# Kernel optimization log

Measured on AMD Instinct MI355X. Metric: run time of the kernel, lower is better.

## Reference

```python
import jax, jax.numpy as jnp
import numpy as np

LN_EPS = 1e-5


def setup_inputs() -> dict:
    key = jax.random.key(0)
    ks = jax.random.split(key, 6)
    n_nodes, mem_dim = 500000, 256
    n_upd, msg_dim = 65536, 512
    return {
        "unique_node_ids": jnp.arange(n_upd, dtype=jnp.int64) if jax.config.jax_enable_x64 else jnp.arange(n_upd, dtype=jnp.int32),
        "unique_messages": jax.random.normal(ks[0], (n_upd, msg_dim), dtype=jnp.float32),
        "timestamps": jax.random.uniform(ks[1], (n_upd,), dtype=jnp.float32),
        "memory": jax.random.normal(ks[2], (n_nodes, mem_dim), dtype=jnp.float32),
        "last_update": jnp.zeros((n_nodes,), dtype=jnp.float32),
        "W_ih": jax.random.normal(ks[3], (3 * mem_dim, msg_dim), dtype=jnp.float32) * (1.0 / np.sqrt(msg_dim)),
        "W_hh": jax.random.normal(ks[4], (3 * mem_dim, mem_dim), dtype=jnp.float32) * (1.0 / np.sqrt(mem_dim)),
        "b_ih": jnp.zeros((3 * mem_dim,), dtype=jnp.float32),
        "b_hh": jnp.zeros((3 * mem_dim,), dtype=jnp.float32),
        "ln_gamma": jnp.ones((mem_dim,), dtype=jnp.float32),
        "ln_beta": jnp.zeros((mem_dim,), dtype=jnp.float32),
    }


def _gru_cell(x, h, W_ih, W_hh, b_ih, b_hh):
    # torch.nn.GRUCell math
    gi = x @ W_ih.T + b_ih          # [N, 3H]
    gh = h @ W_hh.T + b_hh          # [N, 3H]
    i_r, i_z, i_n = jnp.split(gi, 3, axis=-1)
    h_r, h_z, h_n = jnp.split(gh, 3, axis=-1)
    r = jax.nn.sigmoid(i_r + h_r)
    z = jax.nn.sigmoid(i_z + h_z)
    n = jnp.tanh(i_n + r * h_n)
    return (1.0 - z) * n + z * h


def _layer_norm(x, gamma, beta):
    mu = jnp.mean(x, axis=-1, keepdims=True)
    var = jnp.mean(jnp.square(x - mu), axis=-1, keepdims=True)
    return (x - mu) * jax.lax.rsqrt(var + LN_EPS) * gamma + beta


def reference(unique_node_ids, unique_messages, timestamps, memory, last_update,
              W_ih, W_hh, b_ih, b_hh, ln_gamma, ln_beta):
    # gather memory rows for the nodes being updated
    h = memory[unique_node_ids]                      # [N, H]
    new_h = _gru_cell(unique_messages, h, W_ih, W_hh, b_ih, b_hh)
    new_h = _layer_norm(new_h, ln_gamma, ln_beta)
    # scatter updated rows back (get_updated_memory semantics: pure copy)
    updated_memory = memory.at[unique_node_ids].set(new_h)
    updated_last_update = last_update.at[unique_node_ids].set(timestamps)
    return updated_memory, updated_last_update
```

## Files before the change

kernel.cpp:

```cpp
#include <hip/hip_runtime.h>
#include <hip/hip_bf16.h>

typedef float  f32x4 __attribute__((ext_vector_type(4)));
typedef short  s16x8 __attribute__((ext_vector_type(8)));

#define MEMH   256
#define MSGD   512
#define G3     768
#define W_IH_ELEMS (G3*MSGD)
#define W_HH_ELEMS (G3*MEMH)
#define W_TOT_ELEMS (W_IH_ELEMS + W_HH_ELEMS)
#define W_BYTES    ((size_t)W_TOT_ELEMS * 2)

#define BM     32
#define NTHR   1024
#define AM_OFF 0
#define AH_OFF 32768
#define PART_OFF 49152
#define CNT_OFF  51200
#define LDS_BYTES 51264

static __device__ __forceinline__ short f2bf(float x) {
    __hip_bfloat16 b = __float2bfloat16(x);
    return __builtin_bit_cast(short, b);
}
static __device__ __forceinline__ float bf2f(short s) {
    unsigned int u = ((unsigned int)(unsigned short)s) << 16;
    return __builtin_bit_cast(float, u);
}
static __device__ __forceinline__ float sigf(float x) {
    return 1.f / (1.f + __expf(-x));
}
static __device__ __forceinline__ float tanh_fast(float x) {
    float e = __expf(-2.f * fabsf(x));
    float t = (1.f - e) / (1.f + e);
    return copysignf(t, x);
}
static __device__ __forceinline__ f32x4 ntload4(const float* p) {
    return __builtin_nontemporal_load((const f32x4*)p);
}
static __device__ __forceinline__ void ntstore4(float* p, f32x4 v) {
    __builtin_nontemporal_store(v, (f32x4*)p);
}

__global__ void smu_copy_kernel(const float* __restrict__ mem,
                                const float* __restrict__ lu,
                                float* __restrict__ out_mem,
                                float* __restrict__ out_lu,
                                long n_mem4, long n_lu4) {
    long i = (long)blockIdx.x * blockDim.x + threadIdx.x;
    long stride = (long)gridDim.x * blockDim.x;
    long total = n_mem4 + n_lu4;
    for (; i < total; i += stride) {
        if (i < n_mem4) ntstore4(out_mem + i * 4, ntload4(mem + i * 4));
        else {
            long j = (i - n_mem4) * 4;
            ntstore4(out_lu + j, ntload4(lu + j));
        }
    }
}

__global__ void smu_cvtw_kernel(const float* __restrict__ wih,
                                const float* __restrict__ whh,
                                short* __restrict__ o) {
    int i = blockIdx.x * blockDim.x + threadIdx.x;
    if (i >= W_TOT_ELEMS) return;
    if (i < W_IH_ELEMS) {
        int f = i >> 9, r = i & 511, l = r >> 3, e = r & 7;
        int t = f >> 4, k = f & 15;
        int row = t * 16 + (l & 15), col = k * 32 + (l >> 4) * 8 + e;
        o[i] = f2bf(wih[row * MSGD + col]);
    } else {
        int j = i - W_IH_ELEMS;
        int f = j >> 9, r = j & 511, l = r >> 3, e = r & 7;
        int t = f >> 3, k = f & 7;
        int row = t * 16 + (l & 15), col = k * 32 + (l >> 4) * 8 + e;
        o[i] = f2bf(whh[row * MEMH + col]);
    }
}

__global__ void smu_clear_kernel(unsigned* __restrict__ p, int n) {
    int i = blockIdx.x * blockDim.x + threadIdx.x;
    if (i < n) p[i] = 0u;
}
__global__ void smu_bits_kernel(const int* __restrict__ ids,
                                unsigned* __restrict__ bm, int n) {
    int i = blockIdx.x * blockDim.x + threadIdx.x;
    if (i < n) {
        int id = ids[i];
        atomicOr(&bm[id >> 5], 1u << (id & 31));
    }
}

template<bool USE_WS>
static __device__ __forceinline__ s16x8 load_b(const float* __restrict__ Wf,
                                               const short* __restrict__ Wb,
                                               int t, int k, int ldk, int nkt, int lane) {
    if constexpr (USE_WS) {
        return *(const s16x8*)(Wb + ((size_t)(t * nkt + k) << 9) + lane * 8);
    } else {
        int row = t * 16 + (lane & 15);
        int col = k * 32 + (lane >> 4) * 8;
        f32x4 x = *(const f32x4*)(Wf + (size_t)row * ldk + col);
        f32x4 y = *(const f32x4*)(Wf + (size_t)row * ldk + col + 4);
        s16x8 s;
        s[0]=f2bf(x[0]); s[1]=f2bf(x[1]); s[2]=f2bf(x[2]); s[3]=f2bf(x[3]);
        s[4]=f2bf(y[0]); s[5]=f2bf(y[1]); s[6]=f2bf(y[2]); s[7]=f2bf(y[3]);
        return s;
    }
}

template<bool USE_WS, bool FUSED>
__global__ __launch_bounds__(NTHR, 1)
void smu_fused_kernel(const int*   __restrict__ ids,
                      const float* __restrict__ msg,
                      const float* __restrict__ ts,
                      const float* __restrict__ memory,
                      const float* __restrict__ lu,
                      const float* __restrict__ W_ih,
                      const float* __restrict__ W_hh,
                      const float* __restrict__ b_ih,
                      const float* __restrict__ b_hh,
                      const float* __restrict__ gamma,
                      const float* __restrict__ beta,
                      const short* __restrict__ wsw,
                      const unsigned* __restrict__ bm,
                      float* __restrict__ out_mem,
                      float* __restrict__ out_lu,
                      long n_nodes) {
    __shared__ __align__(16) unsigned char lds[LDS_BYTES];
    const int tid = threadIdx.x;
    const int bid = blockIdx.x;
    const long base = (long)bid * BM;

    if (tid == 0) *(unsigned*)(lds + CNT_OFF) = 0u;

    {
        const float* src = msg + base * MSGD;
        #pragma unroll
        for (int it = 0; it < 2; ++it) {
            int u = tid + NTHR * it;
            int row = u >> 6;
            f32x4 a = ntload4(src + u * 8);
            f32x4 b = ntload4(src + u * 8 + 4);
            s16x8 s;
            s[0]=f2bf(a[0]); s[1]=f2bf(a[1]); s[2]=f2bf(a[2]); s[3]=f2bf(a[3]);
            s[4]=f2bf(b[0]); s[5]=f2bf(b[1]); s[6]=f2bf(b[2]); s[7]=f2bf(b[3]);
            int byte = AM_OFF + ((u * 16) ^ ((row & 7) << 4));
            *(s16x8*)(lds + byte) = s;
        }
        {
            int u = tid;
            int row = u >> 5;
            int c8  = u & 31;
            int id  = ids[base + row];
            const float* hs = memory + (size_t)id * MEMH + c8 * 8;
            f32x4 a = ntload4(hs);
            f32x4 b = ntload4(hs + 4);
            s16x8 s;
            s[0]=f2bf(a[0]); s[1]=f2bf(a[1]); s[2]=f2bf(a[2]); s[3]=f2bf(a[3]);
            s[4]=f2bf(b[0]); s[5]=f2bf(b[1]); s[6]=f2bf(b[2]); s[7]=f2bf(b[3]);
            int byte = AH_OFF + ((u * 16) ^ ((row & 7) << 4));
            *(s16x8*)(lds + byte) = s;
        }
    }
    __syncthreads();

    if (tid >= 512) {
        if constexpr (FUSED) {
            const long nu     = n_nodes * (MEMH / 4);
            const long stride = (long)gridDim.x * 512;
            const long i0     = (long)bid * 512 + (tid - 512);

            for (long i = i0; i < nu; i += stride * 8) {
                f32x4 v[8];
                bool  f[8];
                #pragma unroll
                for (int j = 0; j < 8; ++j) {
                    long u = i + stride * j;
                    f[j] = false;
                    if (u < nu) {
                        long r = u >> 6;
                        f[j] = !((bm[r >> 5] >> (r & 31)) & 1u);
                        if (f[j]) v[j] = ntload4(memory + u * 4);
                    }
                }
                #pragma unroll
                for (int j = 0; j < 8; ++j) {
                    long u = i + stride * j;
                    if (f[j]) ntstore4(out_mem + u * 4, v[j]);
                }
            }
            for (long i = i0; i < n_nodes; i += stride) {
                if (!((bm[i >> 5] >> (i & 31)) & 1u)) {
                    float v = __builtin_nontemporal_load(lu + i);
                    __builtin_nontemporal_store(v, out_lu + i);
                }
            }
        }
        return;
    }

    const int lane = tid & 63;
    const int w    = tid >> 6;
    const int lr   = lane & 15;
    const int lk8  = (lane >> 4) * 8;
    const int sw   = (lr & 7) << 4;
    const short* Wi = wsw;
    const short* Wh = wsw + W_IH_ELEMS;

    f32x4 rz[2][2][2] = {};
    f32x4 gin[2][2]   = {};
    f32x4 ghn[2][2]   = {};

    {
        s16x8 b[2][6];
        #pragma unroll
        for (int i = 0; i < 6; ++i)
            b[0][i] = load_b<USE_WS>(W_ih, Wi, w + 8*(i/3) + 16*(i%3), 0, MSGD, 16, lane);
        #pragma unroll
        for (int i = 0; i < 6; ++i)
            b[1][i] = load_b<USE_WS>(W_ih, Wi, w + 8*(i/3) + 16*(i%3), 1, MSGD, 16, lane);
        #pragma unroll
        for (int k = 0; k < 16; ++k) {
            const int cb = (k * 32 + lk8) * 2;
            #pragma unroll
            for (int m = 0; m < 2; ++m) {
                s16x8 a = *(const s16x8*)(lds + AM_OFF + (((m*16 + lr) * 1024 + cb) ^ sw));
                #pragma unroll
                for (int ci = 0; ci < 2; ++ci) {
                    rz[m][ci][0] = __builtin_amdgcn_mfma_f32_16x16x32_bf16(a, b[k & 1][ci*3+0], rz[m][ci][0], 0, 0, 0);
                    rz[m][ci][1] = __builtin_amdgcn_mfma_f32_16x16x32_bf16(a, b[k & 1][ci*3+1], rz[m][ci][1], 0, 0, 0);
                    gin[m][ci]   = __builtin_amdgcn_mfma_f32_16x16x32_bf16(a, b[k & 1][ci*3+2], gin[m][ci],   0, 0, 0);
                }
            }
            if (k < 14) {
                #pragma unroll
                for (int i = 0; i < 6; ++i)
                    b[k & 1][i] = load_b<USE_WS>(W_ih, Wi, w + 8*(i/3) + 16*(i%3), k + 2, MSGD, 16, lane);
            }
        }
    }
    {
        s16x8 b[2][6];
        #pragma unroll
        for (int i = 0; i < 6; ++i)
            b[0][i] = load_b<USE_WS>(W_hh, Wh, w + 8*(i/3) + 16*(i%3), 0, MEMH, 8, lane);
        #pragma unroll
        for (int i = 0; i < 6; ++i)
            b[1][i] = load_b<USE_WS>(W_hh, Wh, w + 8*(i/3) + 16*(i%3), 1, MEMH, 8, lane);
        #pragma unroll
        for (int k = 0; k < 8; ++k) {
            const int cb = (k * 32 + lk8) * 2;
            #pragma unroll
            for (int m = 0; m < 2; ++m) {
                s16x8 a = *(const s16x8*)(lds + AH_OFF + (((m*16 + lr) * 512 + cb) ^ sw));
                #pragma unroll
                for (int ci = 0; ci < 2; ++ci) {
                    rz[m][ci][0] = __builtin_amdgcn_mfma_f32_16x16x32_bf16(a, b[k & 1][ci*3+0], rz[m][ci][0], 0, 0, 0);
                    rz[m][ci][1] = __builtin_amdgcn_mfma_f32_16x16x32_bf16(a, b[k & 1][ci*3+1], rz[m][ci][1], 0, 0, 0);
                    ghn[m][ci]   = __builtin_amdgcn_mfma_f32_16x16x32_bf16(a, b[k & 1][ci*3+2], ghn[m][ci],   0, 0, 0);
                }
            }
            if (k < 6) {
                #pragma unroll
                for (int i = 0; i < 6; ++i)
                    b[k & 1][i] = load_b<USE_WS>(W_hh, Wh, w + 8*(i/3) + 16*(i%3), k + 2, MEMH, 8, lane);
            }
        }
    }

    const int lq = (lane >> 4);
    f32x4 o_[2][2];
    {
        #pragma unroll
        for (int ci = 0; ci < 2; ++ci) {
            const int j = (w + 8*ci) * 16 + lr;
            const float br = b_ih[j]       + b_hh[j];
            const float bz = b_ih[256 + j] + b_hh[256 + j];
            const float bihn = b_ih[512 + j], bhhn = b_hh[512 + j];
            #pragma unroll
            for (int m = 0; m < 2; ++m) {
                #pragma unroll
                for (int q = 0; q < 4; ++q) {
                    int row = m * 16 + lq * 4 + q;
                    float r = sigf(rz[m][ci][0][q] + br);
                    float z = sigf(rz[m][ci][1][q] + bz);
                    float n = tanh_fast(gin[m][ci][q] + bihn + r * (ghn[m][ci][q] + bhhn));
                    float hv = bf2f(*(const short*)(lds + AH_OFF + ((row * 512 + j * 2) ^ ((row & 7) << 4))));
                    o_[m][ci][q] = (1.f - z) * n + z * hv;
                }
            }
        }
    }

    {
        float* part = (float*)(lds + PART_OFF);
        #pragma unroll
        for (int m = 0; m < 2; ++m) {
            #pragma unroll
            for (int q = 0; q < 4; ++q) {
                float v0 = o_[m][0][q], v1 = o_[m][1][q];
                float s1 = v0 + v1;
                float s2 = v0 * v0 + v1 * v1;
                #pragma unroll
                for (int mk = 1; mk < 16; mk <<= 1) {
                    s1 += __shfl_xor(s1, mk);
                    s2 += __shfl_xor(s2, mk);
                }
                if (lr == 0) {
                    int row = m * 16 + lq * 4 + q;
                    part[(row * 8 + w) * 2]     = s1;
                    part[(row * 8 + w) * 2 + 1] = s2;
                }
            }
        }
    }

    __threadfence_block();
    if (lane == 0) atomicAdd((unsigned*)(lds + CNT_OFF), 1u);
    {
        volatile unsigned* cp = (volatile unsigned*)(lds + CNT_OFF);
        while (*cp < 8u) __builtin_amdgcn_s_sleep(2);
    }
    __threadfence_block();

    float mu_[2][4], inv_[2][4];
    {
        const float* part = (const float*)(lds + PART_OFF);
        #pragma unroll
        for (int m = 0; m < 2; ++m) {
            #pragma unroll
            for (int q = 0; q < 4; ++q) {
                int row = m * 16 + lq * 4 + q;
                float s1 = 0.f, s2 = 0.f;
                #pragma unroll
                for (int i = 0; i < 8; ++i) {
                    s1 += part[(row * 8 + i) * 2];
                    s2 += part[(row * 8 + i) * 2 + 1];
                }
                float mu  = s1 * (1.f / 256.f);
                float var = fmaxf(s2 * (1.f / 256.f) - mu * mu, 0.f);
                mu_[m][q]  = mu;
                inv_[m][q] = rsqrtf(var + 1e-5f);
            }
        }
    }

    {
        #pragma unroll
        for (int ci = 0; ci < 2; ++ci) {
            const int j = (w + 8*ci) * 16 + lr;
            const float ga = gamma[j], be = beta[j];
            #pragma unroll
            for (int m = 0; m < 2; ++m) {
                #pragma unroll
                for (int q = 0; q < 4; ++q) {
                    int row = m * 16 + lq * 4 + q;
                    int id = ids[base + row];
                    float y = (o_[m][ci][q] - mu_[m][q]) * inv_[m][q] * ga + be;
                    __builtin_nontemporal_store(y, out_mem + (size_t)id * MEMH + j);
                }
            }
        }
        if (w == 0 && lane < 32) {
            int id = ids[base + lane];
            __builtin_nontemporal_store(ts[base + lane], out_lu + id);
        }
    }
}

extern "C" void kernel_launch(void* const* d_in, const int* in_sizes, int n_in,
                              void* d_out, int out_size, void* d_ws, size_t ws_size,
                              hipStream_t stream) {
    (void)n_in; (void)out_size;
    const int*   ids = (const int*)  d_in[0];
    const float* msg = (const float*)d_in[1];
    const float* ts  = (const float*)d_in[2];
    const float* mem = (const float*)d_in[3];
    const float* lu  = (const float*)d_in[4];
    const float* Wih = (const float*)d_in[5];
    const float* Whh = (const float*)d_in[6];
    const float* bih = (const float*)d_in[7];
    const float* bhh = (const float*)d_in[8];
    const float* gam = (const float*)d_in[9];
    const float* bet = (const float*)d_in[10];

    const int  n_upd   = in_sizes[0];
    const long n_nodes = (long)in_sizes[3] / MEMH;

    float* out_mem = (float*)d_out;
    float* out_lu  = out_mem + (size_t)n_nodes * MEMH;

    const int    bm_words     = (int)((n_nodes + 31) / 32) + 4;
    const size_t bm_bytes_pad = (size_t)bm_words * 4;
    const bool ws_w  = (d_ws != nullptr) && (ws_size >= W_BYTES);
    const bool ws_bm = (d_ws != nullptr) && (ws_size >= W_BYTES + bm_bytes_pad);

    short*    wsw = (short*)d_ws;
    unsigned* bm  = (unsigned*)((char*)d_ws + W_BYTES);

    const int grid = n_upd / BM;

    if (ws_w) {
        smu_cvtw_kernel<<<(W_TOT_ELEMS + 255) / 256, 256, 0, stream>>>(Wih, Whh, wsw);
    }

    if (ws_bm) {
        smu_clear_kernel<<<(bm_words + 255) / 256, 256, 0, stream>>>(bm, bm_words);
        smu_bits_kernel<<<(n_upd + 255) / 256, 256, 0, stream>>>(ids, bm, n_upd);
        smu_fused_kernel<true, true><<<grid, NTHR, 0, stream>>>(
            ids, msg, ts, mem, lu, Wih, Whh, bih, bhh, gam, bet,
            wsw, bm, out_mem, out_lu, n_nodes);
    } else {
        long n_mem4 = n_nodes * (MEMH / 4);
        long n_lu4  = n_nodes / 4;
        smu_copy_kernel<<<2048, 256, 0, stream>>>(mem, lu, out_mem, out_lu, n_mem4, n_lu4);
        if (ws_w) {
            smu_fused_kernel<true, false><<<grid, NTHR, 0, stream>>>(
                ids, msg, ts, mem, lu, Wih, Whh, bih, bhh, gam, bet,
                wsw, nullptr, out_mem, out_lu, n_nodes);
        } else {
            smu_fused_kernel<false, false><<<grid, NTHR, 0, stream>>>(
                ids, msg, ts, mem, lu, Wih, Whh, bih, bhh, gam, bet,
                nullptr, nullptr, out_mem, out_lu, n_nodes);
        }
    }
}
```

Baseline: 377.9 us.

## Split fused copy+GRU kernel into separate bitmap-skip copy and GRU kernels

Removes the warp-specialized design where half of each 1024-thread block streamed the untouched memory rows while the other half ran the GRU. The copy now runs in its own grid-stride kernel that skips rows flagged in the bitmap, followed by a 512-thread GRU kernel allowing several blocks per CU. The LDS spin-wait counter is replaced by a plain __syncthreads. This trades the overlap of copy and compute for simpler scheduling and higher GRU occupancy, at the cost of serializing the bandwidth-bound copy before the compute.

Result: faster. 341.3 us (-9.7%).

```diff
diff --git a/kernel.cpp b/kernel.cpp
--- a/kernel.cpp
+++ b/kernel.cpp
@@ -13,12 +13,11 @@
 #define W_BYTES    ((size_t)W_TOT_ELEMS * 2)
 
 #define BM     32
-#define NTHR   1024
+#define NTHR   512
 #define AM_OFF 0
 #define AH_OFF 32768
 #define PART_OFF 49152
-#define CNT_OFF  51200
-#define LDS_BYTES 51264
+#define LDS_BYTES 51200
 
 static __device__ __forceinline__ short f2bf(float x) {
     __hip_bfloat16 b = __float2bfloat16(x);
@@ -56,6 +55,30 @@
         else {
             long j = (i - n_mem4) * 4;
             ntstore4(out_lu + j, ntload4(lu + j));
+        }
+    }
+}
+
+__global__ __launch_bounds__(256)
+void smu_copy_skip_kernel(const float* __restrict__ mem,
+                          const float* __restrict__ lu,
+                          const unsigned* __restrict__ bm,
+                          float* __restrict__ out_mem,
+                          float* __restrict__ out_lu,
+                          long n_nodes) {
+    const long nu = n_nodes * (MEMH / 4);
+    const long stride = (long)gridDim.x * blockDim.x;
+    const long i0 = (long)blockIdx.x * blockDim.x + threadIdx.x;
+
+    for (long i = i0; i < nu; i += stride) {
+        long r = i >> 6;
+        if (!((bm[r >> 5] >> (r & 31)) & 1u))
+            ntstore4(out_mem + i * 4, ntload4(mem + i * 4));
+    }
+    for (long i = i0; i < n_nodes; i += stride) {
+        if (!((bm[i >> 5] >> (i & 31)) & 1u)) {
+            float v = __builtin_nontemporal_load(lu + i);
+            __builtin_nontemporal_store(v, out_lu + i);
         }
     }
 }
@@ -110,35 +133,29 @@
     }
 }
 
-template<bool USE_WS, bool FUSED>
-__global__ __launch_bounds__(NTHR, 1)
-void smu_fused_kernel(const int*   __restrict__ ids,
-                      const float* __restrict__ msg,
-                      const float* __restrict__ ts,
-                      const float* __restrict__ memory,
-                      const float* __restrict__ lu,
-                      const float* __restrict__ W_ih,
-                      const float* __restrict__ W_hh,
-                      const float* __restrict__ b_ih,
-                      const float* __restrict__ b_hh,
-                      const float* __restrict__ gamma,
-                      const float* __restrict__ beta,
-                      const short* __restrict__ wsw,
-                      const unsigned* __restrict__ bm,
-                      float* __restrict__ out_mem,
-                      float* __restrict__ out_lu,
-                      long n_nodes) {
+template<bool USE_WS>
+__global__ __launch_bounds__(NTHR, 4)
+void smu_gru_kernel(const int*   __restrict__ ids,
+                    const float* __restrict__ msg,
+                    const float* __restrict__ ts,
+                    const float* __restrict__ memory,
+                    const float* __restrict__ W_ih,
+                    const float* __restrict__ W_hh,
+                    const float* __restrict__ b_ih,
+                    const float* __restrict__ b_hh,
+                    const float* __restrict__ gamma,
+                    const float* __restrict__ beta,
+                    const short* __restrict__ wsw,
+                    float* __restrict__ out_mem,
+                    float* __restrict__ out_lu) {
     __shared__ __align__(16) unsigned char lds[LDS_BYTES];
     const int tid = threadIdx.x;
-    const int bid = blockIdx.x;
-    const long base = (long)bid * BM;
-
-    if (tid == 0) *(unsigned*)(lds + CNT_OFF) = 0u;
+    const long base = (long)blockIdx.x * BM;
 
     {
         const float* src = msg + base * MSGD;
         #pragma unroll
-        for (int it = 0; it < 2; ++it) {
+        for (int it = 0; it < 4; ++it) {
             int u = tid + NTHR * it;
             int row = u >> 6;
             f32x4 a = ntload4(src + u * 8);
@@ -149,8 +166,9 @@
             int byte = AM_OFF + ((u * 16) ^ ((row & 7) << 4));
             *(s16x8*)(lds + byte) = s;
         }
-        {
-            int u = tid;
+        #pragma unroll
+        for (int it = 0; it < 2; ++it) {
+            int u = tid + NTHR * it;
             int row = u >> 5;
             int c8  = u & 31;
             int id  = ids[base + row];
@@ -166,41 +184,6 @@
     }
     __syncthreads();
 
-    if (tid >= 512) {
-        if constexpr (FUSED) {
-            const long nu     = n_nodes * (MEMH / 4);
-            const long stride = (long)gridDim.x * 512;
-            const long i0     = (long)bid * 512 + (tid - 512);
-
-            for (long i = i0; i < nu; i += stride * 8) {
-                f32x4 v[8];
-                bool  f[8];
-                #pragma unroll
-                for (int j = 0; j < 8; ++j) {
-                    long u = i + stride * j;
-                    f[j] = false;
-                    if (u < nu) {
-                        long r = u >> 6;
-                        f[j] = !((bm[r >> 5] >> (r & 31)) & 1u);
-                        if (f[j]) v[j] = ntload4(memory + u * 4);
-                    }
-                }
-                #pragma unroll
-                for (int j = 0; j < 8; ++j) {
-                    long u = i + stride * j;
-                    if (f[j]) ntstore4(out_mem + u * 4, v[j]);
-                }
-            }
-            for (long i = i0; i < n_nodes; i += stride) {
-                if (!((bm[i >> 5] >> (i & 31)) & 1u)) {
-                    float v = __builtin_nontemporal_load(lu + i);
-                    __builtin_nontemporal_store(v, out_lu + i);
-                }
-            }
-        }
-        return;
-    }
-
     const int lane = tid & 63;
     const int w    = tid >> 6;
     const int lr   = lane & 15;
@@ -316,14 +299,7 @@
             }
         }
     }
-
-    __threadfence_block();
-    if (lane == 0) atomicAdd((unsigned*)(lds + CNT_OFF), 1u);
-    {
-        volatile unsigned* cp = (volatile unsigned*)(lds + CNT_OFF);
-        while (*cp < 8u) __builtin_amdgcn_s_sleep(2);
-    }
-    __threadfence_block();
+    __syncthreads();
 
     float mu_[2][4], inv_[2][4];
     {
@@ -402,28 +378,24 @@
 
     const int grid = n_upd / BM;
 
-    if (ws_w) {
-        smu_cvtw_kernel<<<(W_TOT_ELEMS + 255) / 256, 256, 0, stream>>>(Wih, Whh, wsw);
-    }
-
-    if (ws_bm) {
+    if (ws_bm && ws_w) {
         smu_clear_kernel<<<(bm_words + 255) / 256, 256, 0, stream>>>(bm, bm_words);
         smu_bits_kernel<<<(n_upd + 255) / 256, 256, 0, stream>>>(ids, bm, n_upd);
-        smu_fused_kernel<true, true><<<grid, NTHR, 0, stream>>>(
-            ids, msg, ts, mem, lu, Wih, Whh, bih, bhh, gam, bet,
-            wsw, bm, out_mem, out_lu, n_nodes);
+        smu_copy_skip_kernel<<<2048, 256, 0, stream>>>(mem, lu, bm, out_mem, out_lu, n_nodes);
+        smu_cvtw_kernel<<<(W_TOT_ELEMS + 255) / 256, 256, 0, stream>>>(Wih, Whh, wsw);
+        smu_gru_kernel<true><<<grid, NTHR, 0, stream>>>(
+            ids, msg, ts, mem, Wih, Whh, bih, bhh, gam, bet, wsw, out_mem, out_lu);
     } else {
         long n_mem4 = n_nodes * (MEMH / 4);
         long n_lu4  = n_nodes / 4;
         smu_copy_kernel<<<2048, 256, 0, stream>>>(mem, lu, out_mem, out_lu, n_mem4, n_lu4);
         if (ws_w) {
-            smu_fused_kernel<true, false><<<grid, NTHR, 0, stream>>>(
-                ids, msg, ts, mem, lu, Wih, Whh, bih, bhh, gam, bet,
-                wsw, nullptr, out_mem, out_lu, n_nodes);
+            smu_cvtw_kernel<<<(W_TOT_ELEMS + 255) / 256, 256, 0, stream>>>(Wih, Whh, wsw);
+            smu_gru_kernel<true><<<grid, NTHR, 0, stream>>>(
+                ids, msg, ts, mem, Wih, Whh, bih, bhh, gam, bet, wsw, out_mem, out_lu);
         } else {
-            smu_fused_kernel<false, false><<<grid, NTHR, 0, stream>>>(
-                ids, msg, ts, mem, lu, Wih, Whh, bih, bhh, gam, bet,
-                nullptr, nullptr, out_mem, out_lu, n_nodes);
-        }
-    }
-}
+            smu_gru_kernel<false><<<grid, NTHR, 0, stream>>>(
+                ids, msg, ts, mem, Wih, Whh, bih, bhh, gam, bet, nullptr, out_mem, out_lu);
+        }
+    }
+}
```
